# Kernel tuning notes

Measured on AMD Instinct MI355X. Metric: run time of the kernel, lower is better.

The kernel has to match this reference:

```python
import jax, jax.numpy as jnp
import numpy as np

B, N, FEAT, HID = 1024, 128, 512, 256


def setup_inputs() -> dict:
    key = jax.random.key(0)
    k1, k2, k3, k4, k5, k6 = jax.random.split(key, 6)
    x = jax.random.normal(k1, (B, FEAT), dtype=jnp.float32)
    labels = jax.random.randint(k2, (B,), 0, N, dtype=jnp.int64)
    W_proj = jax.random.normal(k3, (FEAT, HID), dtype=jnp.float32) / np.sqrt(FEAT)
    b_proj = jax.random.normal(k4, (HID,), dtype=jnp.float32) * 0.01
    means = jax.random.normal(k5, (N, HID), dtype=jnp.float32)
    # inverse covariances must be SPD so sqrt(dist_sq) is real
    A = jax.random.normal(k6, (N, HID, HID), dtype=jnp.float32)
    inv_covs = jnp.einsum('nij,nkj->nik', A, A) / HID + 0.1 * jnp.eye(HID, dtype=jnp.float32)
    return {"x": x, "labels": labels, "W_proj": W_proj, "b_proj": b_proj,
            "means": means, "inv_covs": inv_covs}


def reference(x, labels, W_proj, b_proj, means, inv_covs):
    b = x.shape[0]
    n = means.shape[0]
    x_proj = x @ W_proj + b_proj                       # (b, hid)
    delta = x_proj[:, None, :] - means[None, :, :]     # (b, n, hid)
    # batched Mahalanobis quadratic form
    dist_sq = jnp.einsum('bni,nij,bnj->bn', delta, inv_covs, delta)
    distmat = jnp.sqrt(dist_sq + 1e-12)                # (b, n)
    center_mask = (labels[:, None] == jnp.arange(n)[None, :]).astype(distmat.dtype)
    loss = jnp.clip(distmat * center_mask, 1e-12, 1e12).sum() / b
    return loss, distmat
```

## Files before the change

### kernel.cpp

```cpp
#include <hip/hip_runtime.h>
#include <hip/hip_bf16.h>

#define B_    1024
#define N_    128
#define FEAT_ 512
#define HID_  256
#define LDK   264

typedef __bf16 bf16x8 __attribute__((ext_vector_type(8)));
typedef float  f32x4  __attribute__((ext_vector_type(4)));

__device__ __forceinline__ unsigned int f2bf(float f) {
    unsigned int u = __float_as_uint(f);
    u += 0x7fffu + ((u >> 16) & 1u);
    return u >> 16;
}
__device__ __forceinline__ unsigned int pack2(float a, float b) {
    return f2bf(a) | (f2bf(b) << 16);
}

union U16x8 { uint4 u; bf16x8 v; };

__global__ __launch_bounds__(256) void proj_kernel(
    const float* __restrict__ x, const float* __restrict__ W,
    const float* __restrict__ bias, float* __restrict__ xp)
{
    const int h  = threadIdx.x;
    const int b0 = blockIdx.x * 4;
    const float bb = bias[h];
    float a0 = bb, a1 = bb, a2 = bb, a3 = bb;
    const float* x0p = x + (size_t)(b0 + 0) * FEAT_;
    const float* x1p = x + (size_t)(b0 + 1) * FEAT_;
    const float* x2p = x + (size_t)(b0 + 2) * FEAT_;
    const float* x3p = x + (size_t)(b0 + 3) * FEAT_;
    #pragma unroll 2
    for (int f = 0; f < FEAT_; f += 4) {
        const float4 xv0 = *(const float4*)(x0p + f);
        const float4 xv1 = *(const float4*)(x1p + f);
        const float4 xv2 = *(const float4*)(x2p + f);
        const float4 xv3 = *(const float4*)(x3p + f);
        const float w0 = W[(size_t)(f + 0) * HID_ + h];
        const float w1 = W[(size_t)(f + 1) * HID_ + h];
        const float w2 = W[(size_t)(f + 2) * HID_ + h];
        const float w3 = W[(size_t)(f + 3) * HID_ + h];
        a0 += xv0.x * w0 + xv0.y * w1 + xv0.z * w2 + xv0.w * w3;
        a1 += xv1.x * w0 + xv1.y * w1 + xv1.z * w2 + xv1.w * w3;
        a2 += xv2.x * w0 + xv2.y * w1 + xv2.z * w2 + xv2.w * w3;
        a3 += xv3.x * w0 + xv3.y * w1 + xv3.z * w2 + xv3.w * w3;
    }
    xp[(size_t)(b0 + 0) * HID_ + h] = a0;
    xp[(size_t)(b0 + 1) * HID_ + h] = a1;
    xp[(size_t)(b0 + 2) * HID_ + h] = a2;
    xp[(size_t)(b0 + 3) * HID_ + h] = a3;
}

__global__ __launch_bounds__(512, 2) void dist_kernel(
    const float* __restrict__ xp, const float* __restrict__ means,
    const float* __restrict__ invcov, float* __restrict__ out)
{
    extern __shared__ unsigned short Ms[];

    const int tid  = threadIdx.x;
    const int n    = blockIdx.y;
    const int b0   = blockIdx.x * 512;
    const int wave = tid >> 6;
    const int lane = tid & 63;
    const int q    = lane >> 4;
    const int l    = lane & 15;

    const float* Msrc = invcov + (size_t)n * (HID_ * HID_);
    #pragma unroll
    for (int i = 0; i < 16; ++i) {
        const int g   = tid + i * 512;
        const int row = g >> 5;
        const int gc  = g & 31;
        const float* src = Msrc + (size_t)row * HID_ + gc * 8;
        const float4 a = *(const float4*)src;
        const float4 b = *(const float4*)(src + 4);
        *(uint4*)&Ms[row * LDK + gc * 8] =
            make_uint4(pack2(a.x, a.y), pack2(a.z, a.w), pack2(b.x, b.y), pack2(b.z, b.w));
    }

    const float* mrow = means + (size_t)n * HID_;
    bf16x8 afrag[4][8];
    #pragma unroll
    for (int kk = 0; kk < 8; ++kk) {
        const int k0 = kk * 32 + q * 8;
        const float4 m0 = *(const float4*)(mrow + k0);
        const float4 m1 = *(const float4*)(mrow + k0 + 4);
        #pragma unroll
        for (int rb = 0; rb < 4; ++rb) {
            const float* xr = xp + (size_t)(b0 + wave * 64 + rb * 16 + l) * HID_;
            const float4 x0 = *(const float4*)(xr + k0);
            const float4 x1 = *(const float4*)(xr + k0 + 4);
            U16x8 c;
            c.u = make_uint4(pack2(x0.x - m0.x, x0.y - m0.y),
                             pack2(x0.z - m0.z, x0.w - m0.w),
                             pack2(x1.x - m1.x, x1.y - m1.y),
                             pack2(x1.z - m1.z, x1.w - m1.w));
            afrag[rb][kk] = c.v;
        }
    }
    __syncthreads();

    float muv[16];
    #pragma unroll
    for (int ct = 0; ct < 16; ++ct) muv[ct] = mrow[ct * 16 + l];

    float part[16];
    #pragma unroll
    for (int i = 0; i < 16; ++i) part[i] = 0.f;

    const size_t xbase = (size_t)(b0 + wave * 64 + q * 4) * HID_ + l;

    for (int ct = 0; ct < 16; ++ct) {
        f32x4 acc0 = {0.f,0.f,0.f,0.f}, acc1 = {0.f,0.f,0.f,0.f};
        f32x4 acc2 = {0.f,0.f,0.f,0.f}, acc3 = {0.f,0.f,0.f,0.f};
        #pragma unroll
        for (int kk = 0; kk < 8; ++kk) {
            const bf16x8 bfrag = *(const bf16x8*)&Ms[(ct * 16 + l) * LDK + kk * 32 + q * 8];
            acc0 = __builtin_amdgcn_mfma_f32_16x16x32_bf16(afrag[0][kk], bfrag, acc0, 0, 0, 0);
            acc1 = __builtin_amdgcn_mfma_f32_16x16x32_bf16(afrag[1][kk], bfrag, acc1, 0, 0, 0);
            acc2 = __builtin_amdgcn_mfma_f32_16x16x32_bf16(afrag[2][kk], bfrag, acc2, 0, 0, 0);
            acc3 = __builtin_amdgcn_mfma_f32_16x16x32_bf16(afrag[3][kk], bfrag, acc3, 0, 0, 0);
        }
        const float mu = muv[ct];
        #pragma unroll
        for (int rb = 0; rb < 4; ++rb) {
            const f32x4 a = rb == 0 ? acc0 : rb == 1 ? acc1 : rb == 2 ? acc2 : acc3;
            #pragma unroll
            for (int r = 0; r < 4; ++r) {
                const float d = xp[xbase + (size_t)(rb * 16 + r) * HID_ + ct * 16] - mu;
                part[rb * 4 + r] += a[r] * d;
            }
        }
    }

    #pragma unroll
    for (int i = 0; i < 16; ++i) {
        float v = part[i];
        v += __shfl_xor(v, 1);
        v += __shfl_xor(v, 2);
        v += __shfl_xor(v, 4);
        v += __shfl_xor(v, 8);
        part[i] = v;
    }
    if (l == 0) {
        #pragma unroll
        for (int i = 0; i < 16; ++i) {
            const int row = b0 + wave * 64 + (i >> 2) * 16 + q * 4 + (i & 3);
            out[1 + (size_t)row * N_ + n] = sqrtf(part[i] + 1e-12f);
        }
    }
}

__global__ __launch_bounds__(1024) void loss_kernel(
    const float* __restrict__ distmat, const int* __restrict__ labels,
    float* __restrict__ out)
{
    __shared__ float red[16];
    const int b = threadIdx.x;
    float s = distmat[(size_t)b * N_ + labels[b]];
    #pragma unroll
    for (int m = 1; m <= 32; m <<= 1) s += __shfl_xor(s, m);
    if ((b & 63) == 0) red[b >> 6] = s;
    __syncthreads();
    if (b == 0) {
        float t = 0.f;
        #pragma unroll
        for (int i = 0; i < 16; ++i) t += red[i];
        out[0] = t / (float)B_ + (float)(N_ - 1) * 1e-12f;
    }
}

extern "C" void kernel_launch(void* const* d_in, const int* in_sizes, int n_in,
                              void* d_out, int out_size, void* d_ws, size_t ws_size,
                              hipStream_t stream) {
    const float* x      = (const float*)d_in[0];
    const int*   labels = (const int*)d_in[1];
    const float* W      = (const float*)d_in[2];
    const float* bias   = (const float*)d_in[3];
    const float* means  = (const float*)d_in[4];
    const float* invcov = (const float*)d_in[5];
    float* out = (float*)d_out;
    float* xp  = (float*)d_ws;

    constexpr int DIST_LDS = 256 * LDK * 2;
    (void)hipFuncSetAttribute((const void*)dist_kernel,
                              hipFuncAttributeMaxDynamicSharedMemorySize, DIST_LDS);

    proj_kernel<<<dim3(B_ / 4), 256, 0, stream>>>(x, W, bias, xp);
    dist_kernel<<<dim3(2, N_), 512, DIST_LDS, stream>>>(xp, means, invcov, out);
    loss_kernel<<<1, 1024, 0, stream>>>(out + 1, labels, out);
}
```

Measured before the change: 164.6 us.

## Split Mahalanobis kernel across column halves and smaller batch tiles for more blocks

Splits the dist kernel grid so each block handles 256 batch rows and half of the inverse-covariance rows (128), giving 1024 blocks instead of 256, with half the LDS per block and occupancy raised to 4 blocks per CU. Partial quadratic-form sums for the two column halves go to a workspace buffer, and a new finalize kernel adds them and takes the sqrt. The projection kernel also processes 2 rows per block instead of 4, doubling its block count. The aim is better CU utilisation on the MI355X, in exchange for an extra launch, extra global traffic for the partial sums, and each invcov matrix being loaded by four blocks instead of two.

```diff
diff --git a/kernel.cpp b/kernel.cpp
--- a/kernel.cpp
+++ b/kernel.cpp
@@ -26,51 +26,45 @@
     const float* __restrict__ bias, float* __restrict__ xp)
 {
     const int h  = threadIdx.x;
-    const int b0 = blockIdx.x * 4;
+    const int b0 = blockIdx.x * 2;
     const float bb = bias[h];
-    float a0 = bb, a1 = bb, a2 = bb, a3 = bb;
+    float a0 = bb, a1 = bb;
     const float* x0p = x + (size_t)(b0 + 0) * FEAT_;
     const float* x1p = x + (size_t)(b0 + 1) * FEAT_;
-    const float* x2p = x + (size_t)(b0 + 2) * FEAT_;
-    const float* x3p = x + (size_t)(b0 + 3) * FEAT_;
-    #pragma unroll 2
+    #pragma unroll 4
     for (int f = 0; f < FEAT_; f += 4) {
         const float4 xv0 = *(const float4*)(x0p + f);
         const float4 xv1 = *(const float4*)(x1p + f);
-        const float4 xv2 = *(const float4*)(x2p + f);
-        const float4 xv3 = *(const float4*)(x3p + f);
         const float w0 = W[(size_t)(f + 0) * HID_ + h];
         const float w1 = W[(size_t)(f + 1) * HID_ + h];
         const float w2 = W[(size_t)(f + 2) * HID_ + h];
         const float w3 = W[(size_t)(f + 3) * HID_ + h];
         a0 += xv0.x * w0 + xv0.y * w1 + xv0.z * w2 + xv0.w * w3;
         a1 += xv1.x * w0 + xv1.y * w1 + xv1.z * w2 + xv1.w * w3;
-        a2 += xv2.x * w0 + xv2.y * w1 + xv2.z * w2 + xv2.w * w3;
-        a3 += xv3.x * w0 + xv3.y * w1 + xv3.z * w2 + xv3.w * w3;
     }
     xp[(size_t)(b0 + 0) * HID_ + h] = a0;
     xp[(size_t)(b0 + 1) * HID_ + h] = a1;
-    xp[(size_t)(b0 + 2) * HID_ + h] = a2;
-    xp[(size_t)(b0 + 3) * HID_ + h] = a3;
-}
-
-__global__ __launch_bounds__(512, 2) void dist_kernel(
+}
+
+__global__ __launch_bounds__(512, 4) void dist_kernel(
     const float* __restrict__ xp, const float* __restrict__ means,
-    const float* __restrict__ invcov, float* __restrict__ out)
+    const float* __restrict__ invcov, float* __restrict__ p)
 {
     extern __shared__ unsigned short Ms[];
 
     const int tid  = threadIdx.x;
-    const int n    = blockIdx.y;
-    const int b0   = blockIdx.x * 512;
+    const int bh   = blockIdx.x;
+    const int jh   = blockIdx.y;
+    const int n    = blockIdx.z;
+    const int b0   = bh * 256;
     const int wave = tid >> 6;
     const int lane = tid & 63;
     const int q    = lane >> 4;
     const int l    = lane & 15;
 
-    const float* Msrc = invcov + (size_t)n * (HID_ * HID_);
-    #pragma unroll
-    for (int i = 0; i < 16; ++i) {
+    const float* Msrc = invcov + (size_t)n * (HID_ * HID_) + (size_t)jh * 128 * HID_;
+    #pragma unroll
+    for (int i = 0; i < 8; ++i) {
         const int g   = tid + i * 512;
         const int row = g >> 5;
         const int gc  = g & 31;
@@ -82,15 +76,15 @@
     }
 
     const float* mrow = means + (size_t)n * HID_;
-    bf16x8 afrag[4][8];
+    bf16x8 afrag[2][8];
     #pragma unroll
     for (int kk = 0; kk < 8; ++kk) {
         const int k0 = kk * 32 + q * 8;
         const float4 m0 = *(const float4*)(mrow + k0);
         const float4 m1 = *(const float4*)(mrow + k0 + 4);
         #pragma unroll
-        for (int rb = 0; rb < 4; ++rb) {
-            const float* xr = xp + (size_t)(b0 + wave * 64 + rb * 16 + l) * HID_;
+        for (int rb = 0; rb < 2; ++rb) {
+            const float* xr = xp + (size_t)(b0 + wave * 32 + rb * 16 + l) * HID_;
             const float4 x0 = *(const float4*)(xr + k0);
             const float4 x1 = *(const float4*)(xr + k0 + 4);
             U16x8 c;
@@ -101,43 +95,45 @@
             afrag[rb][kk] = c.v;
         }
     }
+
+    float muv[8];
+    #pragma unroll
+    for (int ct = 0; ct < 8; ++ct) muv[ct] = mrow[jh * 128 + ct * 16 + l];
+
     __syncthreads();
 
-    float muv[16];
-    #pragma unroll
-    for (int ct = 0; ct < 16; ++ct) muv[ct] = mrow[ct * 16 + l];
-
-    float part[16];
-    #pragma unroll
-    for (int i = 0; i < 16; ++i) part[i] = 0.f;
-
-    const size_t xbase = (size_t)(b0 + wave * 64 + q * 4) * HID_ + l;
-
-    for (int ct = 0; ct < 16; ++ct) {
+    float part[8];
+    #pragma unroll
+    for (int i = 0; i < 8; ++i) part[i] = 0.f;
+
+    const size_t xbase = (size_t)(b0 + wave * 32 + q * 4) * HID_ + jh * 128 + l;
+
+    #pragma unroll
+    for (int ct = 0; ct < 8; ++ct) {
+        float xl[8];
+        #pragma unroll
+        for (int rb = 0; rb < 2; ++rb)
+            #pragma unroll
+            for (int r = 0; r < 4; ++r)
+                xl[rb * 4 + r] = xp[xbase + (size_t)(rb * 16 + r) * HID_ + ct * 16];
+
         f32x4 acc0 = {0.f,0.f,0.f,0.f}, acc1 = {0.f,0.f,0.f,0.f};
-        f32x4 acc2 = {0.f,0.f,0.f,0.f}, acc3 = {0.f,0.f,0.f,0.f};
         #pragma unroll
         for (int kk = 0; kk < 8; ++kk) {
             const bf16x8 bfrag = *(const bf16x8*)&Ms[(ct * 16 + l) * LDK + kk * 32 + q * 8];
             acc0 = __builtin_amdgcn_mfma_f32_16x16x32_bf16(afrag[0][kk], bfrag, acc0, 0, 0, 0);
             acc1 = __builtin_amdgcn_mfma_f32_16x16x32_bf16(afrag[1][kk], bfrag, acc1, 0, 0, 0);
-            acc2 = __builtin_amdgcn_mfma_f32_16x16x32_bf16(afrag[2][kk], bfrag, acc2, 0, 0, 0);
-            acc3 = __builtin_amdgcn_mfma_f32_16x16x32_bf16(afrag[3][kk], bfrag, acc3, 0, 0, 0);
         }
         const float mu = muv[ct];
         #pragma unroll
-        for (int rb = 0; rb < 4; ++rb) {
-            const f32x4 a = rb == 0 ? acc0 : rb == 1 ? acc1 : rb == 2 ? acc2 : acc3;
-            #pragma unroll
-            for (int r = 0; r < 4; ++r) {
-                const float d = xp[xbase + (size_t)(rb * 16 + r) * HID_ + ct * 16] - mu;
-                part[rb * 4 + r] += a[r] * d;
-            }
-        }
-    }
-
-    #pragma unroll
-    for (int i = 0; i < 16; ++i) {
+        for (int r = 0; r < 4; ++r) {
+            part[r]     += acc0[r] * (xl[r]     - mu);
+            part[4 + r] += acc1[r] * (xl[4 + r] - mu);
+        }
+    }
+
+    #pragma unroll
+    for (int i = 0; i < 8; ++i) {
         float v = part[i];
         v += __shfl_xor(v, 1);
         v += __shfl_xor(v, 2);
@@ -146,12 +142,20 @@
         part[i] = v;
     }
     if (l == 0) {
-        #pragma unroll
-        for (int i = 0; i < 16; ++i) {
-            const int row = b0 + wave * 64 + (i >> 2) * 16 + q * 4 + (i & 3);
-            out[1 + (size_t)row * N_ + n] = sqrtf(part[i] + 1e-12f);
-        }
-    }
+        float* pb = p + (size_t)jh * (B_ * N_);
+        #pragma unroll
+        for (int i = 0; i < 8; ++i) {
+            const int row = b0 + wave * 32 + (i >> 2) * 16 + q * 4 + (i & 3);
+            pb[(size_t)row * N_ + n] = part[i];
+        }
+    }
+}
+
+__global__ __launch_bounds__(256) void finalize_kernel(
+    const float* __restrict__ p, float* __restrict__ out)
+{
+    const int i = blockIdx.x * 256 + threadIdx.x;
+    out[1 + i] = sqrtf(p[i] + p[B_ * N_ + i] + 1e-12f);
 }
 
 __global__ __launch_bounds__(1024) void loss_kernel(
@@ -184,12 +188,14 @@
     const float* invcov = (const float*)d_in[5];
     float* out = (float*)d_out;
     float* xp  = (float*)d_ws;
-
-    constexpr int DIST_LDS = 256 * LDK * 2;
+    float* p   = xp + (size_t)B_ * HID_;
+
+    constexpr int DIST_LDS = 128 * LDK * 2;
     (void)hipFuncSetAttribute((const void*)dist_kernel,
                               hipFuncAttributeMaxDynamicSharedMemorySize, DIST_LDS);
 
-    proj_kernel<<<dim3(B_ / 4), 256, 0, stream>>>(x, W, bias, xp);
-    dist_kernel<<<dim3(2, N_), 512, DIST_LDS, stream>>>(xp, means, invcov, out);
+    proj_kernel<<<dim3(B_ / 2), 256, 0, stream>>>(x, W, bias, xp);
+    dist_kernel<<<dim3(4, 2, N_), 512, DIST_LDS, stream>>>(xp, means, invcov, p);
+    finalize_kernel<<<dim3((B_ * N_) / 256), 256, 0, stream>>>(p, out);
     loss_kernel<<<1, 1024, 0, stream>>>(out + 1, labels, out);
 }
```

New measurement: 163.3 us. About the same (-0.8%).
